# Optimization experiments

Measured on AMD Instinct MI355X. Metric: run time of the kernel, lower is better.

## Reference

```python
import jax, jax.numpy as jnp
import numpy as np
from jax import lax

K = 3
K2 = K * K
PAD = 1          # dcn padding = kernel_size // 2
OFF_DIL = 2      # offset conv dilation & padding
GN_GROUPS = 32
EPS = 1e-5


def setup_inputs() -> dict:
    key = jax.random.key(0)
    ks = jax.random.split(key, 4)
    B, C1, C2, H, W = 4, 256, 256, 64, 64
    x = jax.random.normal(ks[0], (B, C1, H, W), jnp.float32)
    # offset conv params (zero-init in module; small random here so deformable
    # sampling is genuinely irregular)
    w_off = jax.random.normal(ks[1], (3 * K2, C1, K, K), jnp.float32) * 0.01
    b_off = jax.random.normal(ks[2], (3 * K2,), jnp.float32) * 0.01
    # dcn weight, bias=False
    w_dcn = jax.random.normal(ks[3], (C2, C1, K, K), jnp.float32) * (1.0 / np.sqrt(C1 * K2))
    gamma = jnp.ones((C2,), jnp.float32)
    beta = jnp.zeros((C2,), jnp.float32)
    return {"x": x, "w_off": w_off, "b_off": b_off, "w_dcn": w_dcn,
            "gamma": gamma, "beta": beta}


def _dcnv2_block(x, w_off, b_off, w_dcn, gamma, beta):
    B, C, H, W = x.shape
    C2 = w_dcn.shape[0]

    # ---- offset/mask prediction: 3x3 conv, dilation=2, padding=2, stride=1 ----
    out_off = lax.conv_general_dilated(
        x, w_off, window_strides=(1, 1), padding=[(OFF_DIL, OFF_DIL)] * 2,
        rhs_dilation=(OFF_DIL, OFF_DIL),
        dimension_numbers=("NCHW", "OIHW", "NCHW"))
    out_off = out_off + b_off[None, :, None, None]

    offset = jnp.nan_to_num(jnp.clip(out_off[:, :2 * K2], -64.0, 64.0))
    mask = jax.nn.sigmoid(out_off[:, 2 * K2:])                     # [B,K2,H,W]

    off = offset.reshape(B, K2, 2, H, W)                            # (dy,dx) pairs per kernel pt
    dy, dx = off[:, :, 0], off[:, :, 1]                             # [B,K2,H,W]

    # ---- sampling positions: p0 + pk + offset (stride=1, pad=1, dil=1) ----
    ii = (jnp.arange(K2) // K).astype(jnp.float32)                  # kernel row
    jj = (jnp.arange(K2) % K).astype(jnp.float32)                   # kernel col
    yo = jnp.arange(H, dtype=jnp.float32)
    xo = jnp.arange(W, dtype=jnp.float32)
    py = yo[None, None, :, None] - PAD + ii[None, :, None, None] + dy   # [B,K2,H,W]
    px = xo[None, None, None, :] - PAD + jj[None, :, None, None] + dx

    y0 = jnp.floor(py)
    x0 = jnp.floor(px)
    wy = py - y0                                                    # frac weights
    wx = px - x0
    y0i = y0.astype(jnp.int32)
    x0i = x0.astype(jnp.int32)

    xf = x.reshape(B, C, H * W)

    def gather(yi, xi):
        # zero outside image (torchvision zero-padding bilinear semantics)
        valid = (yi >= 0) & (yi < H) & (xi >= 0) & (xi < W)
        idx = jnp.clip(yi, 0, H - 1) * W + jnp.clip(xi, 0, W - 1)   # [B,K2,H,W]
        v = jax.vmap(lambda xb, ib: xb[:, ib])(xf, idx.reshape(B, -1))  # [B,C,K2*H*W]
        v = v.reshape(B, C, K2, H, W)
        return v * valid[:, None].astype(x.dtype)

    v00 = gather(y0i, x0i)
    v01 = gather(y0i, x0i + 1)
    v10 = gather(y0i + 1, x0i)
    v11 = gather(y0i + 1, x0i + 1)

    wy_ = wy[:, None]
    wx_ = wx[:, None]
    samp = (v00 * (1 - wy_) * (1 - wx_) + v01 * (1 - wy_) * wx_
            + v10 * wy_ * (1 - wx_) + v11 * wy_ * wx_)              # [B,C,K2,H,W]
    samp = samp * mask[:, None]                                     # modulated (DCNv2)

    out = jnp.einsum("bckhw,dck->bdhw", samp, w_dcn.reshape(C2, C, K2))

    # ---- GroupNorm(32, C2) + SiLU ----
    G = GN_GROUPS
    o = out.reshape(B, G, C2 // G, H, W)
    mu = o.mean(axis=(2, 3, 4), keepdims=True)
    var = o.var(axis=(2, 3, 4), keepdims=True)
    o = (o - mu) * lax.rsqrt(var + EPS)
    out = o.reshape(B, C2, H, W) * gamma[None, :, None, None] + beta[None, :, None, None]
    return out * jax.nn.sigmoid(out)


def reference(x, w_off, b_off, w_dcn, gamma, beta):
    return _dcnv2_block(x, w_off, b_off, w_dcn, gamma, beta)
```

## Files before the change

### kernel.cpp

```cpp
#include <hip/hip_runtime.h>
#include <math.h>

#define HW 4096

typedef __attribute__((ext_vector_type(8))) short short8;
typedef __attribute__((ext_vector_type(4))) float f32x4;

static __device__ inline ushort f2bf(float f) {
    uint u = __builtin_bit_cast(uint, f);
    return (ushort)((u + 0x7fffu + ((u >> 16) & 1u)) >> 16);
}
static __device__ inline float bf2f(ushort s) {
    return __builtin_bit_cast(float, (uint)s << 16);
}

__global__ __launch_bounds__(256) void k0_xt(const float* __restrict__ x, ushort* __restrict__ xt)
{
    const int blk = blockIdx.x;
    const int b = blk >> 6, h = blk & 63;
    __shared__ ushort tile[64 * 258];
    const float* xb = x + ((size_t)b * 256) * HW + h * 64;
    const int t = threadIdx.x;
    for (int e = t; e < 16384; e += 256) {
        const int c = e >> 6, j = e & 63;
        tile[j * 258 + c] = f2bf(xb[c * HW + j]);
    }
    __syncthreads();
    uint* xo = (uint*)(xt + ((size_t)b * HW + h * 64) * 256);
    for (int e = t; e < 8192; e += 256) {
        const int j = e >> 7, q = e & 127;
        xo[j * 128 + q] = *(const uint*)&tile[j * 258 + 2 * q];
    }
}

__global__ __launch_bounds__(256) void k0_wt(const float* __restrict__ w_dcn, ushort* __restrict__ wT)
{
    const int d = blockIdx.x;
    __shared__ float wl[2304];
    const int t = threadIdx.x;
    for (int i = t; i < 2304; i += 256) wl[i] = w_dcn[d * 2304 + i];
    __syncthreads();
    for (int i = t; i < 2304; i += 256) {
        const int k = i >> 8, c = i & 255;
        wT[k * 65536 + d * 256 + c] = f2bf(wl[c * 9 + k]);
    }
}

__global__ __launch_bounds__(256) void k0_wo(const float* __restrict__ w_off, ushort* __restrict__ wA)
{
    const int e = blockIdx.x * 256 + threadIdx.x;
    const int k = e >> 13, r = e & 8191;
    const int oc = r >> 8, c = r & 255;
    const float v = (oc < 27) ? w_off[(oc * 256 + c) * 9 + k] : 0.f;
    wA[e] = f2bf(v);
}

__global__ __launch_bounds__(512) void k1_mfma(const ushort* __restrict__ xt,
    const ushort* __restrict__ wA, const float* __restrict__ b_off,
    float* __restrict__ offs, float* __restrict__ mk)
{
    const int bid = blockIdx.x;
    const int b = bid >> 6, h = bid & 63;
    const int t = threadIdx.x;
    const int lane = t & 63, wv = t >> 6;
    const int wq = wv & 3, chalf = wv >> 2;
    const int n = lane & 15, kq = lane >> 4;
    __shared__ float red[4][64][8];

    f32x4 acc0 = {0.f, 0.f, 0.f, 0.f}, acc1 = {0.f, 0.f, 0.f, 0.f};
    const ushort* xb = xt + ((size_t)b * HW) * 256;
    const int cb = chalf * 128;

    for (int k = 0; k < 9; ++k) {
        const int i = k / 3, j = k % 3;
        const int hh = h + 2 * (i - 1);
        if ((unsigned)hh >= 64u) continue;
        const int ww = wq * 16 + n + 2 * (j - 1);
        const bool vw = (unsigned)ww < 64u;
        const ushort* xrow  = xb + (hh * 64 + ww) * 256 + cb + kq * 8;
        const ushort* wrow0 = wA + (k * 32 + n) * 256 + cb + kq * 8;
        const ushort* wrow1 = wrow0 + 16 * 256;
#pragma unroll
        for (int c0 = 0; c0 < 128; c0 += 32) {
            short8 bfv = {0, 0, 0, 0, 0, 0, 0, 0};
            if (vw) bfv = *(const short8*)(xrow + c0);
            const short8 a0 = *(const short8*)(wrow0 + c0);
            const short8 a1 = *(const short8*)(wrow1 + c0);
            acc0 = __builtin_amdgcn_mfma_f32_16x16x32_bf16(a0, bfv, acc0, 0, 0, 0);
            acc1 = __builtin_amdgcn_mfma_f32_16x16x32_bf16(a1, bfv, acc1, 0, 0, 0);
        }
    }

    if (chalf == 1) {
#pragma unroll
        for (int r = 0; r < 4; ++r) {
            red[wq][lane][r]     = acc0[r];
            red[wq][lane][4 + r] = acc1[r];
        }
    }
    __syncthreads();
    if (chalf == 0) {
#pragma unroll
        for (int r = 0; r < 4; ++r) {
            acc0[r] += red[wq][lane][r];
            acc1[r] += red[wq][lane][4 + r];
        }
        const int hw = h * 64 + wq * 16 + n;
#pragma unroll
        for (int r = 0; r < 4; ++r) {
            {
                const int oc = kq * 4 + r;
                float v = acc0[r] + b_off[oc];
                v = fminf(fmaxf(v, -64.f), 64.f);
                offs[(b * 18 + oc) * HW + hw] = v;
            }
            {
                const int oc = 16 + kq * 4 + r;
                const float v = acc1[r] + b_off[min(oc, 26)];
                if (oc < 18) {
                    offs[(b * 18 + oc) * HW + hw] = fminf(fmaxf(v, -64.f), 64.f);
                } else if (oc < 27) {
                    mk[(b * 9 + (oc - 18)) * HW + hw] = 1.f / (1.f + expf(-v));
                }
            }
        }
    }
}

__global__ __launch_bounds__(512) void k2_dcn(const ushort* __restrict__ xt, const ushort* __restrict__ wT,
    const float* __restrict__ offs, const float* __restrict__ mk, float* __restrict__ out)
{
    const int bid = blockIdx.x;
    const int wg = (bid & 7) * 32 + (bid >> 3);
    const int b = wg >> 6, h = wg & 63;
    const int t = threadIdx.x;
    const int lane = t & 63, wv = t >> 6;
    const int n0 = lane & 15, kq = lane >> 4;

    __shared__ __align__(16) ushort S[2][16384];

    const int sw = t >> 3;
    const int so = (t & 7) * 4;
    const int cbyte = (t & 7) * 64;

    const char* xc = (const char*)(xt + ((size_t)b * HW) * 256);
    const float* offb = offs + (size_t)b * 18 * HW + h * 64;
    const float* mkb  = mk   + (size_t)b *  9 * HW + h * 64;

    f32x4 acc[2][4];
#pragma unroll
    for (int dr = 0; dr < 2; ++dr)
#pragma unroll
        for (int nf = 0; nf < 4; ++nf) acc[dr][nf] = (f32x4){0.f, 0.f, 0.f, 0.f};

    auto stage = [&](int k, int pb) {
        const float dy = offb[(2 * k) * HW + sw];
        const float dx = offb[(2 * k + 1) * HW + sw];
        const float mval = mkb[k * HW + sw];
        const float py = (float)(h - 1 + k / 3) + dy;
        const float px = (float)(sw - 1 + k % 3) + dx;
        const float y0f = floorf(py), x0f = floorf(px);
        const float wy = py - y0f, wx = px - x0f;
        const int y0 = (int)y0f, x0 = (int)x0f;
        float w00 = (1.f - wy) * (1.f - wx) * mval, w01 = (1.f - wy) * wx * mval;
        float w10 = wy * (1.f - wx) * mval,         w11 = wy * wx * mval;
        const bool vy0 = (unsigned)y0 < 64u, vy1 = (unsigned)(y0 + 1) < 64u;
        const bool vx0 = (unsigned)x0 < 64u, vx1 = (unsigned)(x0 + 1) < 64u;
        if (!(vy0 && vx0)) w00 = 0.f;
        if (!(vy0 && vx1)) w01 = 0.f;
        if (!(vy1 && vx0)) w10 = 0.f;
        if (!(vy1 && vx1)) w11 = 0.f;
        const int y0c = min(max(y0, 0), 63), y1c = min(max(y0 + 1, 0), 63);
        const int x0c = min(max(x0, 0), 63), x1c = min(max(x0 + 1, 0), 63);
        const int o00 = (y0c * 64 + x0c) * 512, o01 = (y0c * 64 + x1c) * 512;
        const int o10 = (y1c * 64 + x0c) * 512, o11 = (y1c * 64 + x1c) * 512;
#pragma unroll
        for (int j = 0; j < 4; ++j) {
            const int cb2 = cbyte + j * 16;
            const short8 u00 = *(const short8*)(xc + o00 + cb2);
            const short8 u01 = *(const short8*)(xc + o01 + cb2);
            const short8 u10 = *(const short8*)(xc + o10 + cb2);
            const short8 u11 = *(const short8*)(xc + o11 + cb2);
            short8 r;
#pragma unroll
            for (int e = 0; e < 8; ++e) {
                const float v = w00 * bf2f((ushort)u00[e]) + w01 * bf2f((ushort)u01[e])
                              + w10 * bf2f((ushort)u10[e]) + w11 * bf2f((ushort)u11[e]);
                r[e] = (short)f2bf(v);
            }
            const int oct = so + j;
            *(short8*)&S[pb][sw * 256 + ((oct ^ (sw & 7)) << 3)] = r;
        }
    };

    auto gemm = [&](int k, int pb) {
        const ushort* Arow0 = wT + k * 65536 + (wv * 32 + n0) * 256 + kq * 8;
        const ushort* Arow1 = Arow0 + 16 * 256;
#pragma unroll
        for (int c0 = 0; c0 < 256; c0 += 32) {
            const short8 a0 = *(const short8*)(Arow0 + c0);
            const short8 a1 = *(const short8*)(Arow1 + c0);
#pragma unroll
            for (int nf = 0; nf < 4; ++nf) {
                const int w = nf * 16 + n0;
                const int oct = (c0 >> 3) + kq;
                const short8 bf = *(const short8*)&S[pb][w * 256 + ((oct ^ (w & 7)) << 3)];
                acc[0][nf] = __builtin_amdgcn_mfma_f32_16x16x32_bf16(a0, bf, acc[0][nf], 0, 0, 0);
                acc[1][nf] = __builtin_amdgcn_mfma_f32_16x16x32_bf16(a1, bf, acc[1][nf], 0, 0, 0);
            }
        }
    };

    stage(0, 0);
    __syncthreads();
#pragma unroll 1
    for (int k = 0; k < 9; ++k) {
        if (k < 8) stage(k + 1, (k + 1) & 1);
        gemm(k, k & 1);
        __syncthreads();
    }

    float* ob = out + ((size_t)b * 256) * HW + h * 64;
#pragma unroll
    for (int dr = 0; dr < 2; ++dr)
#pragma unroll
        for (int nf = 0; nf < 4; ++nf)
#pragma unroll
            for (int r = 0; r < 4; ++r) {
                const int d = wv * 32 + dr * 16 + kq * 4 + r;
                ob[(size_t)d * HW + nf * 16 + n0] = acc[dr][nf][r];
            }
}

__global__ __launch_bounds__(256) void k3_stats(const float* __restrict__ out, float* __restrict__ stats)
{
    const int bg = blockIdx.x;
    const float* p = out + (size_t)bg * 32768;
    float s = 0.f, s2 = 0.f;
    for (int i = threadIdx.x; i < 8192; i += 256) {
        float4 v = ((const float4*)p)[i];
        s  += v.x + v.y + v.z + v.w;
        s2 += v.x * v.x + v.y * v.y + v.z * v.z + v.w * v.w;
    }
    __shared__ float r1[256], r2[256];
    r1[threadIdx.x] = s; r2[threadIdx.x] = s2;
    __syncthreads();
    for (int st = 128; st > 0; st >>= 1) {
        if (threadIdx.x < st) {
            r1[threadIdx.x] += r1[threadIdx.x + st];
            r2[threadIdx.x] += r2[threadIdx.x + st];
        }
        __syncthreads();
    }
    if (threadIdx.x == 0) {
        const float mean = r1[0] / 32768.f;
        const float var  = r2[0] / 32768.f - mean * mean;
        stats[bg * 2]     = mean;
        stats[bg * 2 + 1] = rsqrtf(var + 1e-5f);
    }
}

__global__ __launch_bounds__(256) void k4_gn(float* __restrict__ out,
    const float* __restrict__ stats, const float* __restrict__ gamma, const float* __restrict__ beta)
{
    const int i4 = blockIdx.x * 256 + threadIdx.x;
    const int elem = i4 << 2;
    const int b = elem >> 20;
    const int ch = (elem >> 12) & 255;
    const int g = ch >> 3;
    const float mean = stats[(b * 32 + g) * 2];
    const float rstd = stats[(b * 32 + g) * 2 + 1];
    const float ga = gamma[ch], be = beta[ch];
    float4 v = ((float4*)out)[i4];
    float vv[4] = {v.x, v.y, v.z, v.w};
#pragma unroll
    for (int j = 0; j < 4; ++j) {
        const float o = (vv[j] - mean) * rstd * ga + be;
        vv[j] = o / (1.f + expf(-o));
    }
    ((float4*)out)[i4] = make_float4(vv[0], vv[1], vv[2], vv[3]);
}

extern "C" void kernel_launch(void* const* d_in, const int* in_sizes, int n_in,
                              void* d_out, int out_size, void* d_ws, size_t ws_size,
                              hipStream_t stream)
{
    const float* x     = (const float*)d_in[0];
    const float* w_off = (const float*)d_in[1];
    const float* b_off = (const float*)d_in[2];
    const float* w_dcn = (const float*)d_in[3];
    const float* gamma = (const float*)d_in[4];
    const float* beta  = (const float*)d_in[5];
    float* out = (float*)d_out;

    ushort* xt    = (ushort*)d_ws;
    float*  offs  = (float*)d_ws + 2097152;
    float*  mk    = offs + 294912;
    float*  stats = mk + 147456;
    ushort* wT    = (ushort*)(stats + 256);
    ushort* wA    = wT + 589824;

    hipLaunchKernelGGL(k0_xt,    dim3(256),  dim3(256), 0, stream, x, xt);
    hipLaunchKernelGGL(k0_wt,    dim3(256),  dim3(256), 0, stream, w_dcn, wT);
    hipLaunchKernelGGL(k0_wo,    dim3(288),  dim3(256), 0, stream, w_off, wA);
    hipLaunchKernelGGL(k1_mfma,  dim3(256),  dim3(512), 0, stream, xt, wA, b_off, offs, mk);
    hipLaunchKernelGGL(k2_dcn,   dim3(256),  dim3(512), 0, stream, xt, wT, offs, mk, out);
    hipLaunchKernelGGL(k3_stats, dim3(128),  dim3(256), 0, stream, out, stats);
    hipLaunchKernelGGL(k4_gn,    dim3(4096), dim3(256), 0, stream, out, stats, gamma, beta);
}
```

Before: 195.9 us.

## Split kernels into half-row blocks, fuse weight prep, precompute bilinear taps

Each kernel now gets more parallelism. The transpose, offset-conv and DCN kernels split each row into two half-width or half-channel blocks, doubling the grid to 512 blocks. The two weight-prep kernels are merged into one launch. The offset conv splits the channel reduction four ways with an LDS reduction. The DCN kernel precomputes bilinear offsets and weights into LDS once per block, and uses packed bf16 conversion with FMAs. Its GEMM is retiled to 64 output channels per wave over 32 columns. Smaller blocks mean less reuse of the weight tiles per block and more redundant weight loads.

```diff
diff --git a/kernel.cpp b/kernel.cpp
--- a/kernel.cpp
+++ b/kernel.cpp
@@ -10,49 +10,48 @@
     uint u = __builtin_bit_cast(uint, f);
     return (ushort)((u + 0x7fffu + ((u >> 16) & 1u)) >> 16);
 }
-static __device__ inline float bf2f(ushort s) {
-    return __builtin_bit_cast(float, (uint)s << 16);
-}
+static __device__ inline float lof(uint u) { return __builtin_bit_cast(float, u << 16); }
+static __device__ inline float hif(uint u) { return __builtin_bit_cast(float, u & 0xffff0000u); }
 
 __global__ __launch_bounds__(256) void k0_xt(const float* __restrict__ x, ushort* __restrict__ xt)
 {
     const int blk = blockIdx.x;
-    const int b = blk >> 6, h = blk & 63;
-    __shared__ ushort tile[64 * 258];
-    const float* xb = x + ((size_t)b * 256) * HW + h * 64;
+    const int b = blk >> 7, h = (blk & 127) >> 1, ch = blk & 1;
+    __shared__ ushort tile[64 * 130];
+    const float* xb = x + ((size_t)(b * 256 + ch * 128)) * HW + h * 64;
     const int t = threadIdx.x;
-    for (int e = t; e < 16384; e += 256) {
+    for (int e = t; e < 8192; e += 256) {
         const int c = e >> 6, j = e & 63;
-        tile[j * 258 + c] = f2bf(xb[c * HW + j]);
-    }
-    __syncthreads();
-    uint* xo = (uint*)(xt + ((size_t)b * HW + h * 64) * 256);
-    for (int e = t; e < 8192; e += 256) {
-        const int j = e >> 7, q = e & 127;
-        xo[j * 128 + q] = *(const uint*)&tile[j * 258 + 2 * q];
-    }
-}
-
-__global__ __launch_bounds__(256) void k0_wt(const float* __restrict__ w_dcn, ushort* __restrict__ wT)
-{
-    const int d = blockIdx.x;
-    __shared__ float wl[2304];
+        tile[j * 130 + c] = f2bf(xb[c * HW + j]);
+    }
+    __syncthreads();
+    for (int e = t; e < 4096; e += 256) {
+        const int j = e >> 6, q = e & 63;
+        uint* xo = (uint*)(xt + ((size_t)b * HW + h * 64 + j) * 256 + ch * 128);
+        xo[q] = *(const uint*)&tile[j * 130 + 2 * q];
+    }
+}
+
+__global__ __launch_bounds__(256) void k0_w(const float* __restrict__ w_dcn,
+    const float* __restrict__ w_off, ushort* __restrict__ wT, ushort* __restrict__ wA)
+{
+    const int bid = blockIdx.x;
     const int t = threadIdx.x;
-    for (int i = t; i < 2304; i += 256) wl[i] = w_dcn[d * 2304 + i];
-    __syncthreads();
-    for (int i = t; i < 2304; i += 256) {
-        const int k = i >> 8, c = i & 255;
-        wT[k * 65536 + d * 256 + c] = f2bf(wl[c * 9 + k]);
-    }
-}
-
-__global__ __launch_bounds__(256) void k0_wo(const float* __restrict__ w_off, ushort* __restrict__ wA)
-{
-    const int e = blockIdx.x * 256 + threadIdx.x;
-    const int k = e >> 13, r = e & 8191;
-    const int oc = r >> 8, c = r & 255;
-    const float v = (oc < 27) ? w_off[(oc * 256 + c) * 9 + k] : 0.f;
-    wA[e] = f2bf(v);
+    if (bid < 256) {
+        const int d = bid;
+        __shared__ float wl[2304];
+        for (int i = t; i < 2304; i += 256) wl[i] = w_dcn[d * 2304 + i];
+        __syncthreads();
+        for (int i = t; i < 2304; i += 256) {
+            const int k = i >> 8, c = i & 255;
+            wT[k * 65536 + d * 256 + c] = f2bf(wl[c * 9 + k]);
+        }
+    } else {
+        const int e = (bid - 256) * 256 + t;
+        const int k = e >> 13, r = e & 8191;
+        const int oc = r >> 8, c = r & 255;
+        wA[e] = f2bf(oc < 27 ? w_off[(oc * 256 + c) * 9 + k] : 0.f);
+    }
 }
 
 __global__ __launch_bounds__(512) void k1_mfma(const ushort* __restrict__ xt,
@@ -60,52 +59,55 @@
     float* __restrict__ offs, float* __restrict__ mk)
 {
     const int bid = blockIdx.x;
-    const int b = bid >> 6, h = bid & 63;
+    const int b = bid >> 7, rr_ = bid & 127, h = rr_ >> 1, wh = rr_ & 1;
     const int t = threadIdx.x;
     const int lane = t & 63, wv = t >> 6;
-    const int wq = wv & 3, chalf = wv >> 2;
+    const int wq = wv & 1, cq = wv >> 1;
     const int n = lane & 15, kq = lane >> 4;
-    __shared__ float red[4][64][8];
+    __shared__ float red[2][3][64][8];
 
     f32x4 acc0 = {0.f, 0.f, 0.f, 0.f}, acc1 = {0.f, 0.f, 0.f, 0.f};
     const ushort* xb = xt + ((size_t)b * HW) * 256;
-    const int cb = chalf * 128;
-
+    const int wcol = wh * 32 + wq * 16 + n;
+    const int cb = cq * 64 + kq * 8;
+
+#pragma unroll
     for (int k = 0; k < 9; ++k) {
         const int i = k / 3, j = k % 3;
         const int hh = h + 2 * (i - 1);
-        if ((unsigned)hh >= 64u) continue;
-        const int ww = wq * 16 + n + 2 * (j - 1);
-        const bool vw = (unsigned)ww < 64u;
-        const ushort* xrow  = xb + (hh * 64 + ww) * 256 + cb + kq * 8;
-        const ushort* wrow0 = wA + (k * 32 + n) * 256 + cb + kq * 8;
-        const ushort* wrow1 = wrow0 + 16 * 256;
-#pragma unroll
-        for (int c0 = 0; c0 < 128; c0 += 32) {
-            short8 bfv = {0, 0, 0, 0, 0, 0, 0, 0};
-            if (vw) bfv = *(const short8*)(xrow + c0);
-            const short8 a0 = *(const short8*)(wrow0 + c0);
-            const short8 a1 = *(const short8*)(wrow1 + c0);
-            acc0 = __builtin_amdgcn_mfma_f32_16x16x32_bf16(a0, bfv, acc0, 0, 0, 0);
-            acc1 = __builtin_amdgcn_mfma_f32_16x16x32_bf16(a1, bfv, acc1, 0, 0, 0);
-        }
-    }
-
-    if (chalf == 1) {
+        const int ww = wcol + 2 * (j - 1);
+        const bool ok = ((unsigned)hh < 64u) && ((unsigned)ww < 64u);
+        const int hc = min(max(hh, 0), 63), wc = min(max(ww, 0), 63);
+        const ushort* xrow = xb + (hc * 64 + wc) * 256 + cb;
+        const ushort* wr0 = wA + (k * 32 + n) * 256 + cb;
+#pragma unroll
+        for (int c0 = 0; c0 < 64; c0 += 32) {
+            short8 bv = *(const short8*)(xrow + c0);
+            if (!ok) bv = (short8){0, 0, 0, 0, 0, 0, 0, 0};
+            const short8 a0 = *(const short8*)(wr0 + c0);
+            const short8 a1 = *(const short8*)(wr0 + 16 * 256 + c0);
+            acc0 = __builtin_amdgcn_mfma_f32_16x16x32_bf16(a0, bv, acc0, 0, 0, 0);
+            acc1 = __builtin_amdgcn_mfma_f32_16x16x32_bf16(a1, bv, acc1, 0, 0, 0);
+        }
+    }
+
+    if (cq > 0) {
 #pragma unroll
         for (int r = 0; r < 4; ++r) {
-            red[wq][lane][r]     = acc0[r];
-            red[wq][lane][4 + r] = acc1[r];
-        }
-    }
-    __syncthreads();
-    if (chalf == 0) {
-#pragma unroll
-        for (int r = 0; r < 4; ++r) {
-            acc0[r] += red[wq][lane][r];
-            acc1[r] += red[wq][lane][4 + r];
-        }
-        const int hw = h * 64 + wq * 16 + n;
+            red[wq][cq - 1][lane][r]     = acc0[r];
+            red[wq][cq - 1][lane][4 + r] = acc1[r];
+        }
+    }
+    __syncthreads();
+    if (cq == 0) {
+#pragma unroll
+        for (int p = 0; p < 3; ++p)
+#pragma unroll
+            for (int r = 0; r < 4; ++r) {
+                acc0[r] += red[wq][p][lane][r];
+                acc1[r] += red[wq][p][lane][4 + r];
+            }
+        const int hw = h * 64 + wcol;
 #pragma unroll
         for (int r = 0; r < 4; ++r) {
             {
@@ -127,38 +129,28 @@
     }
 }
 
-__global__ __launch_bounds__(512) void k2_dcn(const ushort* __restrict__ xt, const ushort* __restrict__ wT,
+__global__ __launch_bounds__(256) void k2_dcn(const ushort* __restrict__ xt, const ushort* __restrict__ wT,
     const float* __restrict__ offs, const float* __restrict__ mk, float* __restrict__ out)
 {
     const int bid = blockIdx.x;
-    const int wg = (bid & 7) * 32 + (bid >> 3);
-    const int b = wg >> 6, h = wg & 63;
+    const int wg = (bid & 7) * 64 + (bid >> 3);
+    const int b = wg >> 7, h = (wg & 127) >> 1, wh = wg & 1;
     const int t = threadIdx.x;
     const int lane = t & 63, wv = t >> 6;
     const int n0 = lane & 15, kq = lane >> 4;
-
-    __shared__ __align__(16) ushort S[2][16384];
-
-    const int sw = t >> 3;
-    const int so = (t & 7) * 4;
-    const int cbyte = (t & 7) * 64;
-
-    const char* xc = (const char*)(xt + ((size_t)b * HW) * 256);
-    const float* offb = offs + (size_t)b * 18 * HW + h * 64;
-    const float* mkb  = mk   + (size_t)b *  9 * HW + h * 64;
-
-    f32x4 acc[2][4];
-#pragma unroll
-    for (int dr = 0; dr < 2; ++dr)
-#pragma unroll
-        for (int nf = 0; nf < 4; ++nf) acc[dr][nf] = (f32x4){0.f, 0.f, 0.f, 0.f};
-
-    auto stage = [&](int k, int pb) {
-        const float dy = offb[(2 * k) * HW + sw];
-        const float dx = offb[(2 * k + 1) * HW + sw];
-        const float mval = mkb[k * HW + sw];
+    const int d0 = wv * 64;
+
+    __shared__ __align__(16) ushort S[2][8192];
+    __shared__ int4   cOff[288];
+    __shared__ float4 cWgt[288];
+
+    for (int e = t; e < 288; e += 256) {
+        const int k = e >> 5, sl = e & 31, w = wh * 32 + sl;
+        const float dy = offs[((size_t)b * 18 + 2 * k) * HW + h * 64 + w];
+        const float dx = offs[((size_t)b * 18 + 2 * k + 1) * HW + h * 64 + w];
+        const float mval = mk[((size_t)b * 9 + k) * HW + h * 64 + w];
         const float py = (float)(h - 1 + k / 3) + dy;
-        const float px = (float)(sw - 1 + k % 3) + dx;
+        const float px = (float)(w - 1 + k % 3) + dx;
         const float y0f = floorf(py), x0f = floorf(px);
         const float wy = py - y0f, wx = px - x0f;
         const int y0 = (int)y0f, x0 = (int)x0f;
@@ -172,45 +164,76 @@
         if (!(vy1 && vx1)) w11 = 0.f;
         const int y0c = min(max(y0, 0), 63), y1c = min(max(y0 + 1, 0), 63);
         const int x0c = min(max(x0, 0), 63), x1c = min(max(x0 + 1, 0), 63);
-        const int o00 = (y0c * 64 + x0c) * 512, o01 = (y0c * 64 + x1c) * 512;
-        const int o10 = (y1c * 64 + x0c) * 512, o11 = (y1c * 64 + x1c) * 512;
+        cOff[e] = make_int4((y0c * 64 + x0c) * 512, (y0c * 64 + x1c) * 512,
+                            (y1c * 64 + x0c) * 512, (y1c * 64 + x1c) * 512);
+        cWgt[e] = make_float4(w00, w01, w10, w11);
+    }
+
+    f32x4 acc[4][2];
+#pragma unroll
+    for (int df = 0; df < 4; ++df)
+#pragma unroll
+        for (int nf = 0; nf < 2; ++nf) acc[df][nf] = (f32x4){0.f, 0.f, 0.f, 0.f};
+
+    const char* xc = (const char*)(xt + ((size_t)b * HW) * 256);
+    const int sl = t >> 3, tj = t & 7;
+    const int w7 = sl & 7;
+
+    auto stage = [&](int k, int pb) {
+        const int4   co = cOff[k * 32 + sl];
+        const float4 cw = cWgt[k * 32 + sl];
+        ushort* Sr = &S[pb][sl * 256];
 #pragma unroll
         for (int j = 0; j < 4; ++j) {
-            const int cb2 = cbyte + j * 16;
-            const short8 u00 = *(const short8*)(xc + o00 + cb2);
-            const short8 u01 = *(const short8*)(xc + o01 + cb2);
-            const short8 u10 = *(const short8*)(xc + o10 + cb2);
-            const short8 u11 = *(const short8*)(xc + o11 + cb2);
-            short8 r;
-#pragma unroll
-            for (int e = 0; e < 8; ++e) {
-                const float v = w00 * bf2f((ushort)u00[e]) + w01 * bf2f((ushort)u01[e])
-                              + w10 * bf2f((ushort)u10[e]) + w11 * bf2f((ushort)u11[e]);
-                r[e] = (short)f2bf(v);
-            }
-            const int oct = so + j;
-            *(short8*)&S[pb][sw * 256 + ((oct ^ (sw & 7)) << 3)] = r;
+            const int oct = tj + 8 * j;
+            const int cb2 = oct * 16;
+            const uint4 v00 = *(const uint4*)(xc + co.x + cb2);
+            const uint4 v01 = *(const uint4*)(xc + co.y + cb2);
+            const uint4 v10 = *(const uint4*)(xc + co.z + cb2);
+            const uint4 v11 = *(const uint4*)(xc + co.w + cb2);
+            const uint a00[4] = {v00.x, v00.y, v00.z, v00.w};
+            const uint a01[4] = {v01.x, v01.y, v01.z, v01.w};
+            const uint a10[4] = {v10.x, v10.y, v10.z, v10.w};
+            const uint a11[4] = {v11.x, v11.y, v11.z, v11.w};
+            uint r[4];
+#pragma unroll
+            for (int q = 0; q < 4; ++q) {
+                float lo = cw.x * lof(a00[q]);
+                lo = fmaf(cw.y, lof(a01[q]), lo);
+                lo = fmaf(cw.z, lof(a10[q]), lo);
+                lo = fmaf(cw.w, lof(a11[q]), lo);
+                float hi = cw.x * hif(a00[q]);
+                hi = fmaf(cw.y, hif(a01[q]), hi);
+                hi = fmaf(cw.z, hif(a10[q]), hi);
+                hi = fmaf(cw.w, hif(a11[q]), hi);
+                asm("v_cvt_pk_bf16_f32 %0, %1, %2" : "=v"(r[q]) : "v"(lo), "v"(hi));
+            }
+            uint4 rv = {r[0], r[1], r[2], r[3]};
+            *(uint4*)(Sr + ((oct ^ w7) << 3)) = rv;
         }
     };
 
     auto gemm = [&](int k, int pb) {
-        const ushort* Arow0 = wT + k * 65536 + (wv * 32 + n0) * 256 + kq * 8;
-        const ushort* Arow1 = Arow0 + 16 * 256;
+        const ushort* A = wT + k * 65536 + (d0 + n0) * 256 + kq * 8;
 #pragma unroll
         for (int c0 = 0; c0 < 256; c0 += 32) {
-            const short8 a0 = *(const short8*)(Arow0 + c0);
-            const short8 a1 = *(const short8*)(Arow1 + c0);
-#pragma unroll
-            for (int nf = 0; nf < 4; ++nf) {
-                const int w = nf * 16 + n0;
-                const int oct = (c0 >> 3) + kq;
-                const short8 bf = *(const short8*)&S[pb][w * 256 + ((oct ^ (w & 7)) << 3)];
-                acc[0][nf] = __builtin_amdgcn_mfma_f32_16x16x32_bf16(a0, bf, acc[0][nf], 0, 0, 0);
-                acc[1][nf] = __builtin_amdgcn_mfma_f32_16x16x32_bf16(a1, bf, acc[1][nf], 0, 0, 0);
+            short8 a[4];
+#pragma unroll
+            for (int df = 0; df < 4; ++df)
+                a[df] = *(const short8*)(A + df * 4096 + c0);
+            const int g0 = (c0 >> 3) + kq;
+#pragma unroll
+            for (int nf = 0; nf < 2; ++nf) {
+                const int wl = nf * 16 + n0;
+                const short8 bf = *(const short8*)&S[pb][wl * 256 + ((g0 ^ (wl & 7)) << 3)];
+#pragma unroll
+                for (int df = 0; df < 4; ++df)
+                    acc[df][nf] = __builtin_amdgcn_mfma_f32_16x16x32_bf16(a[df], bf, acc[df][nf], 0, 0, 0);
             }
         }
     };
 
+    __syncthreads();
     stage(0, 0);
     __syncthreads();
 #pragma unroll 1
@@ -220,15 +243,15 @@
         __syncthreads();
     }
 
-    float* ob = out + ((size_t)b * 256) * HW + h * 64;
-#pragma unroll
-    for (int dr = 0; dr < 2; ++dr)
-#pragma unroll
-        for (int nf = 0; nf < 4; ++nf)
+    float* ob = out + ((size_t)b * 256) * HW + h * 64 + wh * 32;
+#pragma unroll
+    for (int df = 0; df < 4; ++df)
+#pragma unroll
+        for (int nf = 0; nf < 2; ++nf)
 #pragma unroll
             for (int r = 0; r < 4; ++r) {
-                const int d = wv * 32 + dr * 16 + kq * 4 + r;
-                ob[(size_t)d * HW + nf * 16 + n0] = acc[dr][nf][r];
+                const int d = d0 + df * 16 + kq * 4 + r;
+                ob[(size_t)d * HW + nf * 16 + n0] = acc[df][nf][r];
             }
 }
 
@@ -300,11 +323,10 @@
     ushort* wT    = (ushort*)(stats + 256);
     ushort* wA    = wT + 589824;
 
-    hipLaunchKernelGGL(k0_xt,    dim3(256),  dim3(256), 0, stream, x, xt);
-    hipLaunchKernelGGL(k0_wt,    dim3(256),  dim3(256), 0, stream, w_dcn, wT);
-    hipLaunchKernelGGL(k0_wo,    dim3(288),  dim3(256), 0, stream, w_off, wA);
-    hipLaunchKernelGGL(k1_mfma,  dim3(256),  dim3(512), 0, stream, xt, wA, b_off, offs, mk);
-    hipLaunchKernelGGL(k2_dcn,   dim3(256),  dim3(512), 0, stream, xt, wT, offs, mk, out);
+    hipLaunchKernelGGL(k0_xt,    dim3(512),  dim3(256), 0, stream, x, xt);
+    hipLaunchKernelGGL(k0_w,     dim3(544),  dim3(256), 0, stream, w_dcn, w_off, wT, wA);
+    hipLaunchKernelGGL(k1_mfma,  dim3(512),  dim3(512), 0, stream, xt, wA, b_off, offs, mk);
+    hipLaunchKernelGGL(k2_dcn,   dim3(512),  dim3(256), 0, stream, xt, wT, offs, mk, out);
     hipLaunchKernelGGL(k3_stats, dim3(128),  dim3(256), 0, stream, out, stats);
     hipLaunchKernelGGL(k4_gn,    dim3(4096), dim3(256), 0, stream, out, stats, gamma, beta);
 }
```

New measurement: 204.2 us. +4.3%, slower.
